# Performance work log

Hardware: AMD Instinct MI355X
Metric: run time of the kernel (lower is better)

## Reference

```python
import jax, jax.numpy as jnp
import numpy as np

KS = 3
OFF = (KS - 1) // 2
KS2 = KS * KS


def _windows(xp, H, W):
    """xp: [..., H+KS-1, W+KS-1] -> [..., H, W, KS, KS] with flat index i = x*KS + y."""
    cols = [xp[..., x:x + H, y:y + W] for x in range(KS) for y in range(KS)]
    w = jnp.stack(cols, axis=-1)                      # [..., H, W, KS*KS]
    return w.reshape(w.shape[:-1] + (KS, KS))


def setup_inputs() -> dict:
    key = jax.random.key(0)
    k1, k2, k3, k4 = jax.random.split(key, 4)
    B, C, H = 8, 3, 512
    img = jax.random.uniform(k1, (B, C, H, H), dtype=jnp.float32) * 255.0
    noise = jax.random.uniform(k2, (B, C, H + 2 * OFF, H + 2 * OFF), dtype=jnp.float32)
    ids_sel = jax.random.randint(k3, (B,), 0, 2) > 0          # ~p selection mask
    ids_dilation_sel = jax.random.randint(k4, (B,), 0, 2) > 0  # ~p_mix mix mask
    return {"img": img, "noise": noise, "ids_sel": ids_sel,
            "ids_dilation_sel": ids_dilation_sel}


def reference(img, noise, ids_sel, ids_dilation_sel):
    B, C, H, W = img.shape
    imgf = img.astype(jnp.float32)
    # pad + additive uniform noise
    img_p = jnp.pad(imgf, ((0, 0), (0, 0), (OFF, OFF), (OFF, OFF))) + noise
    img_e = _windows(img_p, H, W)                     # [B,C,H,W,KS,KS]
    mean = img_e.mean(axis=(4, 5), keepdims=True)
    std = jnp.std(img_e, axis=(4, 5), ddof=1, keepdims=True)  # unbiased
    w = jnp.exp(-(img_e - mean) ** 2 / (2.0 * std ** 2))
    w3 = w.min(axis=1, keepdims=True)                 # [B,1,H,W,KS,KS]
    # first weighted average (sums channels in numerator, like the torch code)
    num = (img_e * w3).sum(axis=(1, 4, 5))            # [B,H,W]
    den = w3.sum(axis=(4, 5))[:, 0]                   # [B,H,W]
    img_r = num / den
    # sort-based pixel mixing: pick argmin (erosion) or argmax (dilation) index
    img_r_p = jnp.pad(img_r, ((0, 0), (OFF, OFF), (OFF, OFF)))
    img_r_e = _windows(img_r_p, H, W).reshape(B, H, W, KS2)
    ids_min = jnp.argmin(img_r_e, axis=3)
    ids_max = jnp.argmax(img_r_e, axis=3)
    ids_mix = jnp.where(ids_dilation_sel[:, None, None], ids_max, ids_min)
    w_flat = w3.reshape(B, H, W, KS2)
    w_mod = jnp.take_along_axis(w_flat, ids_mix[..., None], axis=3)[..., 0]  # [B,H,W]
    # second windowed weighted-average pass with the mixed weights
    w_mod_p = jnp.pad(w_mod, ((0, 0), (OFF, OFF), (OFF, OFF)))
    w_mod_e = _windows(w_mod_p, H, W)[:, None]        # [B,1,H,W,KS,KS]
    img_mod = (img_e * w_mod_e).sum(axis=(4, 5)) / w_mod_e.sum(axis=(4, 5))  # [B,C,H,W]
    out = jnp.where(ids_sel[:, None, None, None], img_mod, imgf)
    return out.astype(jnp.uint8)
```

## Files before the change

### kernel.cpp

```cpp
#include <hip/hip_runtime.h>
#include <hip/hip_fp16.h>

#define HH 512
#define WD 512
#define HP 514
#define BN 8
#define CN 3

#define TH 16
#define TW 32

#define SP_ROWS (TH + 6)
#define SP_COLS (TW + 6)
#define SR_ROWS (TH + 4)
#define SR_COLS (TW + 4)
#define SR_PITCH (SR_COLS + 1)
#define WM_ROWS (TH + 2)
#define WM_COLS (TW + 2)
#define WM_PITCH (WM_COLS + 1)
#define W9_STRIDE 10

__device__ __forceinline__ int load_flag(const int* __restrict__ p, int b) {
    bool all01 = true;
#pragma unroll
    for (int i = 0; i < BN; ++i) {
        int v = p[i];
        all01 = all01 && (v == 0 || v == 1);
    }
    if (all01) return p[b];
    const unsigned char* pb = (const unsigned char*)p;
    return pb[b] != 0;
}

__device__ __forceinline__ float fast_rcp(float x) {
    return __builtin_amdgcn_rcpf(x);
}

__global__ __launch_bounds__(256) void fused(const float* __restrict__ img,
                                             const float* __restrict__ noise,
                                             const int* __restrict__ ids_sel,
                                             const int* __restrict__ ids_dil,
                                             int* __restrict__ out) {
    int b = blockIdx.z;
    int h0 = blockIdx.y * TH, w0 = blockIdx.x * TW;
    int t = threadIdx.x;

    if (!load_flag(ids_sel, b)) {
#pragma unroll
        for (int c = 0; c < CN; ++c) {
            const float* im = img + (size_t)(b * CN + c) * HH * WD;
            int* op = out + (size_t)(b * CN + c) * HH * WD;
#pragma unroll
            for (int rr = 0; rr < (TH * TW) / 256; ++rr) {
                int idx = rr * 256 + t;
                int r = idx / TW, cc = idx - r * TW;
                op[(h0 + r) * WD + w0 + cc] = ((int)im[(h0 + r) * WD + w0 + cc]) & 255;
            }
        }
        return;
    }
    bool dil = load_flag(ids_dil, b) != 0;

    __shared__ float4 sp4[SP_ROWS * SP_COLS];
    __shared__ float sr[SR_ROWS * SR_PITCH];
    __shared__ float swm[WM_ROWS * WM_PITCH];
    __shared__ __align__(4) __half w9[WM_ROWS * WM_COLS * W9_STRIDE];

    {
        const float* nz = noise + (size_t)b * CN * HP * HP;
        const float* im = img + (size_t)b * CN * HH * WD;
        for (int idx = t; idx < SP_ROWS * SP_COLS; idx += 256) {
            int r = idx / SP_COLS, cc = idx - r * SP_COLS;
            int ip = h0 - 2 + r, jp = w0 - 2 + cc;
            ip = ip < 0 ? 0 : (ip > HP - 1 ? HP - 1 : ip);
            jp = jp < 0 ? 0 : (jp > HP - 1 ? HP - 1 : jp);
            bool in = (ip >= 1 && ip <= HH && jp >= 1 && jp <= WD);
            int no = ip * HP + jp;
            int io = (ip - 1) * WD + (jp - 1);
            float4 v;
            v.x = nz[no] + (in ? im[io] : 0.f);
            v.y = nz[HP * HP + no] + (in ? im[HH * WD + io] : 0.f);
            v.z = nz[2 * HP * HP + no] + (in ? im[2 * HH * WD + io] : 0.f);
            v.w = 0.f;
            sp4[idx] = v;
        }
    }
    __syncthreads();

    for (int idx = t; idx < SR_ROWS * SR_COLS; idx += 256) {
        int r = idx / SR_COLS, cc = idx - r * SR_COLS;
        int h = h0 - 2 + r, w = w0 - 2 + cc;
        float val = 0.f;
        if (h >= 0 && h < HH && w >= 0 && w < WD) {
            float4 tp[9];
#pragma unroll
            for (int k = 0; k < 9; ++k)
                tp[k] = sp4[(r + k / 3) * SP_COLS + cc + k % 3];
            float sx = 0.f, sy = 0.f, sz = 0.f;
#pragma unroll
            for (int k = 0; k < 9; ++k) { sx += tp[k].x; sy += tp[k].y; sz += tp[k].z; }
            float mx = sx * (1.f / 9.f), my = sy * (1.f / 9.f), mz = sz * (1.f / 9.f);
            float sdx = 0.f, sdy = 0.f, sdz = 0.f;
#pragma unroll
            for (int k = 0; k < 9; ++k) {
                float dx = tp[k].x - mx, dy = tp[k].y - my, dz = tp[k].z - mz;
                sdx += dx * dx; sdy += dy * dy; sdz += dz * dz;
            }
            float ivx = 4.f * fast_rcp(sdx);
            float ivy = 4.f * fast_rcp(sdy);
            float ivz = 4.f * fast_rcp(sdz);
            float wk[9];
            float num = 0.f, den = 0.f;
#pragma unroll
            for (int k = 0; k < 9; ++k) {
                float dx = tp[k].x - mx, dy = tp[k].y - my, dz = tp[k].z - mz;
                float txx = dx * dx * ivx, tyy = dy * dy * ivy, tzz = dz * dz * ivz;
                float m = fmaxf(txx, fmaxf(tyy, tzz));
                wk[k] = __expf(-m);
                num += (tp[k].x + tp[k].y + tp[k].z) * wk[k];
                den += wk[k];
            }
            val = num * fast_rcp(den);
            if (r >= 1 && r < SR_ROWS - 1 && cc >= 1 && cc < SR_COLS - 1) {
                int pix = (r - 1) * WM_COLS + (cc - 1);
                unsigned int* wp = (unsigned int*)&w9[pix * W9_STRIDE];
#pragma unroll
                for (int k = 0; k < 4; ++k) {
                    __half2 h2 = __floats2half2_rn(wk[2 * k], wk[2 * k + 1]);
                    wp[k] = *(unsigned int*)&h2;
                }
                w9[pix * W9_STRIDE + 8] = __float2half_rn(wk[8]);
            }
        }
        sr[r * SR_PITCH + cc] = val;
    }
    __syncthreads();

    for (int idx = t; idx < WM_ROWS * WM_COLS; idx += 256) {
        int r = idx / WM_COLS, cc = idx - r * WM_COLS;
        int h = h0 - 1 + r, w = w0 - 1 + cc;
        float wmv = 0.f;
        if (h >= 0 && h < HH && w >= 0 && w < WD) {
            float rv[9];
#pragma unroll
            for (int k = 0; k < 9; ++k)
                rv[k] = sr[(r + k / 3) * SR_PITCH + cc + k % 3];
            int amin = 0, amax = 0;
            float vmin = rv[0], vmax = rv[0];
#pragma unroll
            for (int k = 1; k < 9; ++k) {
                if (rv[k] < vmin) { vmin = rv[k]; amin = k; }
                if (rv[k] > vmax) { vmax = rv[k]; amax = k; }
            }
            int ksel = dil ? amax : amin;
            wmv = __half2float(w9[idx * W9_STRIDE + ksel]);
        }
        swm[r * WM_PITCH + cc] = wmv;
    }
    __syncthreads();

#pragma unroll
    for (int rr = 0; rr < (TH * TW) / 256; ++rr) {
        int idx = rr * 256 + t;
        int ly = idx / TW, lx = idx - ly * TW;
        float wk[9], den = 0.f;
#pragma unroll
        for (int k = 0; k < 9; ++k) {
            wk[k] = swm[(ly + k / 3) * WM_PITCH + lx + k % 3];
            den += wk[k];
        }
        float rden = 1.f / den;
        float nx = 0.f, ny = 0.f, nz2 = 0.f;
#pragma unroll
        for (int k = 0; k < 9; ++k) {
            float4 tp = sp4[(ly + 2 + k / 3) * SP_COLS + lx + 2 + k % 3];
            nx += tp.x * wk[k];
            ny += tp.y * wk[k];
            nz2 += tp.z * wk[k];
        }
        size_t o = ((size_t)b * CN * HH + h0 + ly) * WD + w0 + lx;
        out[o] = ((int)(nx * rden)) & 255;
        out[o + (size_t)HH * WD] = ((int)(ny * rden)) & 255;
        out[o + 2 * (size_t)HH * WD] = ((int)(nz2 * rden)) & 255;
    }
}

extern "C" void kernel_launch(void* const* d_in, const int* in_sizes, int n_in,
                              void* d_out, int out_size, void* d_ws, size_t ws_size,
                              hipStream_t stream) {
    const float* img   = (const float*)d_in[0];
    const float* noise = (const float*)d_in[1];
    const int* ids_sel = (const int*)d_in[2];
    const int* ids_dil = (const int*)d_in[3];
    int* out = (int*)d_out;

    dim3 grid(WD / TW, HH / TH, BN);
    fused<<<grid, 256, 0, stream>>>(img, noise, ids_sel, ids_dil, out);
}
```

Baseline: 112.9 us.

## Remap blocks across XCDs, reuse sliding-window registers, vectorize nontemporal stores

Block indices are remapped so each XCD handles a contiguous band of tiles per batch image, aiming at better L2 locality for shared halos. The first stage now has each thread compute three adjacent pixels and slide a 3x3 float4 column window in registers, cutting redundant LDS reads. The final stage has each thread compute two adjacent output pixels and reuse loaded columns and weights. Output writes, including the copy path, become 64-bit nontemporal stores. This adds register pressure and idles 16 threads in the first stage.

```diff
diff --git a/kernel.cpp b/kernel.cpp
--- a/kernel.cpp
+++ b/kernel.cpp
@@ -36,26 +36,85 @@
     return __builtin_amdgcn_rcpf(x);
 }
 
+template <int P>
+__device__ __forceinline__ void p2_pixel(const float4 (&col)[3][3], int r, int cc,
+                                         bool hok, int w,
+                                         float* __restrict__ sr,
+                                         __half* __restrict__ w9) {
+    float val = 0.f;
+    if (hok && (unsigned)w < (unsigned)WD) {
+        float sx = 0.f, sy = 0.f, sz = 0.f;
+#pragma unroll
+        for (int k = 0; k < 9; ++k) {
+            const float4 tp = col[(k % 3 + P) % 3][k / 3];
+            sx += tp.x; sy += tp.y; sz += tp.z;
+        }
+        float mx = sx * (1.f / 9.f), my = sy * (1.f / 9.f), mz = sz * (1.f / 9.f);
+        float sdx = 0.f, sdy = 0.f, sdz = 0.f;
+#pragma unroll
+        for (int k = 0; k < 9; ++k) {
+            const float4 tp = col[(k % 3 + P) % 3][k / 3];
+            float dx = tp.x - mx, dy = tp.y - my, dz = tp.z - mz;
+            sdx += dx * dx; sdy += dy * dy; sdz += dz * dz;
+        }
+        float ivx = 4.f * fast_rcp(sdx);
+        float ivy = 4.f * fast_rcp(sdy);
+        float ivz = 4.f * fast_rcp(sdz);
+        float wk[9];
+        float num = 0.f, den = 0.f;
+#pragma unroll
+        for (int k = 0; k < 9; ++k) {
+            const float4 tp = col[(k % 3 + P) % 3][k / 3];
+            float dx = tp.x - mx, dy = tp.y - my, dz = tp.z - mz;
+            float txx = dx * dx * ivx, tyy = dy * dy * ivy, tzz = dz * dz * ivz;
+            float m = fmaxf(txx, fmaxf(tyy, tzz));
+            wk[k] = __expf(-m);
+            num += (tp.x + tp.y + tp.z) * wk[k];
+            den += wk[k];
+        }
+        val = num * fast_rcp(den);
+        if (r >= 1 && r < SR_ROWS - 1 && cc >= 1 && cc < SR_COLS - 1) {
+            int pix = (r - 1) * WM_COLS + (cc - 1);
+            unsigned int* wp = (unsigned int*)&w9[pix * W9_STRIDE];
+#pragma unroll
+            for (int k = 0; k < 4; ++k) {
+                __half2 h2 = __floats2half2_rn(wk[2 * k], wk[2 * k + 1]);
+                wp[k] = *(unsigned int*)&h2;
+            }
+            w9[pix * W9_STRIDE + 8] = __float2half_rn(wk[8]);
+        }
+    }
+    sr[r * SR_PITCH + cc] = val;
+}
+
 __global__ __launch_bounds__(256) void fused(const float* __restrict__ img,
                                              const float* __restrict__ noise,
                                              const int* __restrict__ ids_sel,
                                              const int* __restrict__ ids_dil,
                                              int* __restrict__ out) {
-    int b = blockIdx.z;
-    int h0 = blockIdx.y * TH, w0 = blockIdx.x * TW;
+    int lin = blockIdx.x + 16 * blockIdx.y + 512 * blockIdx.z;
+    int xcd = lin & 7;
+    int m = lin >> 3;
+    int b = m >> 6;
+    int within = m & 63;
+    int band = (xcd + b) & 7;
+    int tl = band * 64 + within;
+    int by = tl >> 4, bx = tl & 15;
+    int h0 = by * TH, w0 = bx * TW;
     int t = threadIdx.x;
 
     if (!load_flag(ids_sel, b)) {
+        int r = t >> 4, lx = (t & 15) << 1;
 #pragma unroll
         for (int c = 0; c < CN; ++c) {
             const float* im = img + (size_t)(b * CN + c) * HH * WD;
             int* op = out + (size_t)(b * CN + c) * HH * WD;
-#pragma unroll
-            for (int rr = 0; rr < (TH * TW) / 256; ++rr) {
-                int idx = rr * 256 + t;
-                int r = idx / TW, cc = idx - r * TW;
-                op[(h0 + r) * WD + w0 + cc] = ((int)im[(h0 + r) * WD + w0 + cc]) & 255;
-            }
+            float2 v = *(const float2*)&im[(h0 + r) * WD + w0 + lx];
+            int2 ov;
+            ov.x = ((int)v.x) & 255;
+            ov.y = ((int)v.y) & 255;
+            __builtin_nontemporal_store(*(const long long*)&ov,
+                                        (long long*)&op[(h0 + r) * WD + w0 + lx]);
         }
         return;
     }
@@ -87,52 +146,25 @@
     }
     __syncthreads();
 
-    for (int idx = t; idx < SR_ROWS * SR_COLS; idx += 256) {
-        int r = idx / SR_COLS, cc = idx - r * SR_COLS;
-        int h = h0 - 2 + r, w = w0 - 2 + cc;
-        float val = 0.f;
-        if (h >= 0 && h < HH && w >= 0 && w < WD) {
-            float4 tp[9];
-#pragma unroll
-            for (int k = 0; k < 9; ++k)
-                tp[k] = sp4[(r + k / 3) * SP_COLS + cc + k % 3];
-            float sx = 0.f, sy = 0.f, sz = 0.f;
-#pragma unroll
-            for (int k = 0; k < 9; ++k) { sx += tp[k].x; sy += tp[k].y; sz += tp[k].z; }
-            float mx = sx * (1.f / 9.f), my = sy * (1.f / 9.f), mz = sz * (1.f / 9.f);
-            float sdx = 0.f, sdy = 0.f, sdz = 0.f;
-#pragma unroll
-            for (int k = 0; k < 9; ++k) {
-                float dx = tp[k].x - mx, dy = tp[k].y - my, dz = tp[k].z - mz;
-                sdx += dx * dx; sdy += dy * dy; sdz += dz * dz;
-            }
-            float ivx = 4.f * fast_rcp(sdx);
-            float ivy = 4.f * fast_rcp(sdy);
-            float ivz = 4.f * fast_rcp(sdz);
-            float wk[9];
-            float num = 0.f, den = 0.f;
-#pragma unroll
-            for (int k = 0; k < 9; ++k) {
-                float dx = tp[k].x - mx, dy = tp[k].y - my, dz = tp[k].z - mz;
-                float txx = dx * dx * ivx, tyy = dy * dy * ivy, tzz = dz * dz * ivz;
-                float m = fmaxf(txx, fmaxf(tyy, tzz));
-                wk[k] = __expf(-m);
-                num += (tp[k].x + tp[k].y + tp[k].z) * wk[k];
-                den += wk[k];
-            }
-            val = num * fast_rcp(den);
-            if (r >= 1 && r < SR_ROWS - 1 && cc >= 1 && cc < SR_COLS - 1) {
-                int pix = (r - 1) * WM_COLS + (cc - 1);
-                unsigned int* wp = (unsigned int*)&w9[pix * W9_STRIDE];
-#pragma unroll
-                for (int k = 0; k < 4; ++k) {
-                    __half2 h2 = __floats2half2_rn(wk[2 * k], wk[2 * k + 1]);
-                    wp[k] = *(unsigned int*)&h2;
-                }
-                w9[pix * W9_STRIDE + 8] = __float2half_rn(wk[8]);
-            }
-        }
-        sr[r * SR_PITCH + cc] = val;
+    if (t < 240) {
+        int r = t / 12;
+        int s = t - r * 12;
+        int cc0 = 3 * s;
+        int h = h0 - 2 + r;
+        bool hok = (h >= 0 && h < HH);
+        float4 col[3][3];
+#pragma unroll
+        for (int j = 0; j < 3; ++j)
+#pragma unroll
+            for (int i = 0; i < 3; ++i)
+                col[j][i] = sp4[(r + i) * SP_COLS + cc0 + j];
+        p2_pixel<0>(col, r, cc0 + 0, hok, w0 - 2 + cc0 + 0, sr, w9);
+#pragma unroll
+        for (int i = 0; i < 3; ++i) col[0][i] = sp4[(r + i) * SP_COLS + cc0 + 3];
+        p2_pixel<1>(col, r, cc0 + 1, hok, w0 - 2 + cc0 + 1, sr, w9);
+#pragma unroll
+        for (int i = 0; i < 3; ++i) col[1][i] = sp4[(r + i) * SP_COLS + cc0 + 4];
+        p2_pixel<2>(col, r, cc0 + 2, hok, w0 - 2 + cc0 + 2, sr, w9);
     }
     __syncthreads();
 
@@ -159,29 +191,58 @@
     }
     __syncthreads();
 
-#pragma unroll
-    for (int rr = 0; rr < (TH * TW) / 256; ++rr) {
-        int idx = rr * 256 + t;
-        int ly = idx / TW, lx = idx - ly * TW;
-        float wk[9], den = 0.f;
-#pragma unroll
-        for (int k = 0; k < 9; ++k) {
-            wk[k] = swm[(ly + k / 3) * WM_PITCH + lx + k % 3];
-            den += wk[k];
-        }
-        float rden = 1.f / den;
-        float nx = 0.f, ny = 0.f, nz2 = 0.f;
-#pragma unroll
-        for (int k = 0; k < 9; ++k) {
-            float4 tp = sp4[(ly + 2 + k / 3) * SP_COLS + lx + 2 + k % 3];
-            nx += tp.x * wk[k];
-            ny += tp.y * wk[k];
-            nz2 += tp.z * wk[k];
+    {
+        int ly = t >> 4;
+        int lx = (t & 15) << 1;
+        float4 c4[3][3];
+#pragma unroll
+        for (int j = 0; j < 3; ++j)
+#pragma unroll
+            for (int i = 0; i < 3; ++i)
+                c4[j][i] = sp4[(ly + 2 + i) * SP_COLS + lx + 2 + j];
+        float ws[4][3];
+#pragma unroll
+        for (int j = 0; j < 4; ++j)
+#pragma unroll
+            for (int i = 0; i < 3; ++i)
+                ws[j][i] = swm[(ly + i) * WM_PITCH + lx + j];
+        int2 o0, o1, o2;
+        {
+            float den = 0.f, nx = 0.f, ny = 0.f, nz2 = 0.f;
+#pragma unroll
+            for (int k = 0; k < 9; ++k) {
+                const float wkk = ws[k % 3][k / 3];
+                const float4 tp = c4[k % 3][k / 3];
+                den += wkk;
+                nx += tp.x * wkk; ny += tp.y * wkk; nz2 += tp.z * wkk;
+            }
+            float rden = 1.f / den;
+            o0.x = ((int)(nx * rden)) & 255;
+            o1.x = ((int)(ny * rden)) & 255;
+            o2.x = ((int)(nz2 * rden)) & 255;
+        }
+#pragma unroll
+        for (int i = 0; i < 3; ++i) c4[0][i] = sp4[(ly + 2 + i) * SP_COLS + lx + 5];
+        {
+            float den = 0.f, nx = 0.f, ny = 0.f, nz2 = 0.f;
+#pragma unroll
+            for (int k = 0; k < 9; ++k) {
+                const float wkk = ws[k % 3 + 1][k / 3];
+                const float4 tp = c4[(k % 3 + 1) % 3][k / 3];
+                den += wkk;
+                nx += tp.x * wkk; ny += tp.y * wkk; nz2 += tp.z * wkk;
+            }
+            float rden = 1.f / den;
+            o0.y = ((int)(nx * rden)) & 255;
+            o1.y = ((int)(ny * rden)) & 255;
+            o2.y = ((int)(nz2 * rden)) & 255;
         }
         size_t o = ((size_t)b * CN * HH + h0 + ly) * WD + w0 + lx;
-        out[o] = ((int)(nx * rden)) & 255;
-        out[o + (size_t)HH * WD] = ((int)(ny * rden)) & 255;
-        out[o + 2 * (size_t)HH * WD] = ((int)(nz2 * rden)) & 255;
+        __builtin_nontemporal_store(*(const long long*)&o0, (long long*)&out[o]);
+        __builtin_nontemporal_store(*(const long long*)&o1,
+                                    (long long*)&out[o + (size_t)HH * WD]);
+        __builtin_nontemporal_store(*(const long long*)&o2,
+                                    (long long*)&out[o + 2 * (size_t)HH * WD]);
     }
 }
 
```

Measured after the change: 110.8 us. Within noise of the previous version (-1.8%).
